# Kernel tuning notes

Measured on AMD Instinct MI355X. Metric: run time of the kernel, lower is better.

## Reference

```python
import jax, jax.numpy as jnp
import numpy as np

NEG_INF = -9e15  # matches -9000000000000000.0 in the torch source


def setup_inputs() -> dict:
    key = jax.random.key(0)
    k1, k2, k3, k4 = jax.random.split(key, 4)
    B, H, N, D = 4, 8, 2048, 64
    queries = jax.random.normal(k1, (B, H, N, D), dtype=jnp.float32)
    keys = jax.random.normal(k2, (B, H, N, D), dtype=jnp.float32)
    values = jax.random.normal(k3, (B, H, N, D), dtype=jnp.float32)
    adj = jax.random.randint(k4, (N, N), 0, 2, dtype=jnp.int32)
    return {"queries": queries, "keys": keys, "values": values, "adj": adj}


def reference(queries, keys, values, adj):
    B, H, N, D = queries.shape
    # e = Q K^T / 8  (hard-coded divisor == sqrt(64))
    e = jnp.einsum("bhnd,bhmd->bhnm", queries, keys) / 8.0
    # graph-adjacency mask (adj [N,N] broadcasts over batch and heads)
    att = jnp.where(adj > 0, e, NEG_INF)
    att = jax.nn.softmax(att, axis=-1)
    # dropout p=0.0 / eval mode -> identity
    h_prime = jnp.einsum("bhnm,bhmd->bhnd", att, values)  # [B,H,N,D]
    # original uses .view (flat reshape), NOT a permute
    return h_prime.reshape(N, B, H, D)
```

## Files before the change

### kernel.cpp

```cpp
#include <hip/hip_runtime.h>
#include <math.h>

typedef short short8 __attribute__((ext_vector_type(8)));
typedef float float4_t __attribute__((ext_vector_type(4)));
typedef unsigned uint2_t __attribute__((ext_vector_type(2)));
typedef unsigned short ushort_t;

#define BH   32
#define N_   2048
#define D_   64
#define NCH  32
#define LDP  72
#define KV_ELEMS (BH * N_ * D_)
#define OFF_VF  (KV_ELEMS * 2)
#define OFF_MSK (KV_ELEMS * 4)
#define QSCALE 0.18033688f

__device__ __forceinline__ unsigned pack_bf16(float a, float b) {
  union { float f; unsigned u; } ua{a}, ub{b};
  return __builtin_amdgcn_perm(ub.u + 0x8000u, ua.u + 0x8000u, 0x07060302u);
}

__global__ __launch_bounds__(256) void prep_kernel(
    const float* __restrict__ K, const float* __restrict__ V,
    const int* __restrict__ adj, ushort_t* __restrict__ Kf,
    ushort_t* __restrict__ Vf, unsigned long long* __restrict__ msk) {
  __shared__ __align__(16) float Tc[64 * 68];
  const int blk = blockIdx.x, t = threadIdx.x;

  if (blk < 2048) {
    const bool isK = blk < 1024;
    const int b = isK ? blk : blk - 1024;
    const float* src = (isK ? K : V) + (b >> 5) * (N_ * D_) + (b & 31) * 64 * D_;
#pragma unroll
    for (int i = 0; i < 4; ++i) {
      int idx = i * 256 + t;
      int row = idx >> 4, c4 = (idx & 15) * 4;
      *(float4_t*)&Tc[row * 68 + c4] = *(const float4_t*)(src + row * D_ + c4);
    }
    __syncthreads();
    ushort_t* dst = (isK ? Kf : Vf) + b * 4096;
#pragma unroll
    for (int e = 0; e < 2; ++e) {
      int u = t * 2 + e;
      int g = u >> 6, lane = u & 63;
      int ks = g >> 2, quad = lane >> 4, l16 = lane & 15;
      float v[8];
      if (isK) {
        int nt = g & 3;
        const float* rp = &Tc[(nt * 16 + l16) * 68 + ks * 32 + quad * 8];
        float4_t a = *(const float4_t*)(rp);
        float4_t bq = *(const float4_t*)(rp + 4);
#pragma unroll
        for (int j = 0; j < 4; ++j) { v[j] = a[j]; v[4 + j] = bq[j]; }
      } else {
        int dt = g & 3, d = dt * 16 + l16;
#pragma unroll
        for (int j = 0; j < 8; ++j) {
          int key = 16 * (j & 3) + ks * 8 + quad * 2 + (j >> 2);
          v[j] = Tc[key * 68 + d];
        }
      }
      union { short8 s; unsigned u4[4]; } h;
      h.u4[0] = pack_bf16(v[0], v[1]); h.u4[1] = pack_bf16(v[2], v[3]);
      h.u4[2] = pack_bf16(v[4], v[5]); h.u4[3] = pack_bf16(v[6], v[7]);
      *(short8*)(dst + u * 8) = h.s;
    }
  } else {
    const int row = (blk - 2048) * 4 + (t >> 6);
    const int lane = t & 63;
    unsigned long long keep = 0;
#pragma unroll 8
    for (int i = 0; i < 32; ++i) {
      int a = adj[row * N_ + i * 64 + lane];
      unsigned long long b = __ballot(a > 0);
      if (lane == i) keep = b;
    }
    if (lane < 32) msk[row * 32 + lane] = keep;
  }
}

__global__ __launch_bounds__(256, 2) void attn_main(
    const float* __restrict__ Q, const ushort_t* __restrict__ Kf,
    const ushort_t* __restrict__ Vf, const unsigned long long* __restrict__ msk,
    float* __restrict__ O) {
  __shared__ __align__(16) ushort_t lds_p[4][2][16 * LDP];

  const int t    = threadIdx.x;
  const int w    = t >> 6;
  const int lane = t & 63;
  const int quad = lane >> 4;
  const int l16  = lane & 15;
  const int bh   = blockIdx.x & (BH - 1);
  const int qt   = blockIdx.x >> 5;
  const int base = bh * (N_ * D_);
  const int qrow0 = qt * 128 + w * 32;

  const ushort_t* Kfb = Kf + (bh * 32) * 4096;
  const ushort_t* Vfb = Vf + (bh * 32) * 4096;
  const unsigned long long* mr[2] = {
    msk + (qrow0 + quad * 4) * 32,
    msk + (qrow0 + 16 + quad * 4) * 32
  };

  short8 qf[2][2];
#pragma unroll
  for (int qg = 0; qg < 2; ++qg)
#pragma unroll
    for (int ks = 0; ks < 2; ++ks) {
      const float* qp = Q + base + (qrow0 + qg * 16 + l16) * D_ + ks * 32 + quad * 8;
      float4_t f0 = *(const float4_t*)(qp);
      float4_t f1 = *(const float4_t*)(qp + 4);
      union { short8 s; unsigned u[4]; } h;
      h.u[0] = pack_bf16(f0[0] * QSCALE, f0[1] * QSCALE);
      h.u[1] = pack_bf16(f0[2] * QSCALE, f0[3] * QSCALE);
      h.u[2] = pack_bf16(f1[0] * QSCALE, f1[1] * QSCALE);
      h.u[3] = pack_bf16(f1[2] * QSCALE, f1[3] * QSCALE);
      qf[qg][ks] = h.s;
    }

  short8 ones;
#pragma unroll
  for (int j = 0; j < 8; ++j) ones[j] = (short)0x3F80;

  float4_t oacc[2][4];
  float4_t osum[2];
#pragma unroll
  for (int qg = 0; qg < 2; ++qg) {
#pragma unroll
    for (int dt = 0; dt < 4; ++dt) oacc[qg][dt] = (float4_t){0.f, 0.f, 0.f, 0.f};
    osum[qg] = (float4_t){0.f, 0.f, 0.f, 0.f};
  }

  const int fo = lane * 8;

  for (int c = 0; c < NCH; ++c) {
    const ushort_t* kg = Kfb + c * 4096;
    const ushort_t* vg = Vfb + c * 4096;

    short8 kfr[2][4], vfr[2][4];
#pragma unroll
    for (int ks = 0; ks < 2; ++ks)
#pragma unroll
      for (int nt = 0; nt < 4; ++nt) {
        kfr[ks][nt] = *(const short8*)(kg + (ks * 4 + nt) * 512 + fo);
        vfr[ks][nt] = *(const short8*)(vg + (ks * 4 + nt) * 512 + fo);
      }
    unsigned long long mw[2][4];
#pragma unroll
    for (int qg = 0; qg < 2; ++qg)
#pragma unroll
      for (int r = 0; r < 4; ++r) mw[qg][r] = mr[qg][r * 32 + c];

#pragma unroll
    for (int qg = 0; qg < 2; ++qg) {
      float4_t sacc[4];
#pragma unroll
      for (int nt = 0; nt < 4; ++nt) sacc[nt] = (float4_t){0.f, 0.f, 0.f, 0.f};
#pragma unroll
      for (int ks = 0; ks < 2; ++ks)
#pragma unroll
        for (int nt = 0; nt < 4; ++nt)
          sacc[nt] = __builtin_amdgcn_mfma_f32_16x16x32_bf16(qf[qg][ks], kfr[ks][nt], sacc[nt], 0, 0, 0);

#pragma unroll
      for (int r = 0; r < 4; ++r) {
        unsigned long long sh = mw[qg][r] >> l16;
        unsigned lo = (unsigned)sh, hi = (unsigned)(sh >> 32);
        float p0 = (lo & 1u)       ? exp2f(sacc[0][r]) : 0.f;
        float p1 = (lo & 0x10000u) ? exp2f(sacc[1][r]) : 0.f;
        float p2 = (hi & 1u)       ? exp2f(sacc[2][r]) : 0.f;
        float p3 = (hi & 0x10000u) ? exp2f(sacc[3][r]) : 0.f;
        uint2_t d2;
        d2.x = pack_bf16(p0, p1);
        d2.y = pack_bf16(p2, p3);
        *(uint2_t*)&lds_p[w][qg][(quad * 4 + r) * LDP + (l16 << 2)] = d2;
      }
    }

#pragma unroll
    for (int qg = 0; qg < 2; ++qg)
#pragma unroll
      for (int ks = 0; ks < 2; ++ks) {
        short8 pf = *(const short8*)&lds_p[w][qg][l16 * LDP + ks * 32 + quad * 8];
#pragma unroll
        for (int dt = 0; dt < 4; ++dt)
          oacc[qg][dt] = __builtin_amdgcn_mfma_f32_16x16x32_bf16(pf, vfr[ks][dt], oacc[qg][dt], 0, 0, 0);
        osum[qg] = __builtin_amdgcn_mfma_f32_16x16x32_bf16(pf, ones, osum[qg], 0, 0, 0);
      }
  }

#pragma unroll
  for (int qg = 0; qg < 2; ++qg)
#pragma unroll
    for (int r = 0; r < 4; ++r) {
      float inv = 1.f / osum[qg][r];
      int qi = qrow0 + qg * 16 + quad * 4 + r;
#pragma unroll
      for (int dt = 0; dt < 4; ++dt)
        O[base + qi * D_ + dt * 16 + l16] = oacc[qg][dt][r] * inv;
    }
}

extern "C" void kernel_launch(void* const* d_in, const int* in_sizes, int n_in,
                              void* d_out, int out_size, void* d_ws, size_t ws_size,
                              hipStream_t stream) {
  const float* Q  = (const float*)d_in[0];
  const float* K  = (const float*)d_in[1];
  const float* V  = (const float*)d_in[2];
  const int* adj  = (const int*)d_in[3];
  float* O        = (float*)d_out;
  ushort_t* Kf    = (ushort_t*)d_ws;
  ushort_t* Vf    = (ushort_t*)((char*)d_ws + OFF_VF);
  unsigned long long* msk = (unsigned long long*)((char*)d_ws + OFF_MSK);

  prep_kernel<<<2560, 256, 0, stream>>>(K, V, adj, Kf, Vf, msk);
  attn_main<<<512, 256, 0, stream>>>(Q, Kf, Vf, msk, O);
}
```

Baseline: 184.3 us.

## Double-buffer K/V chunks in LDS via async global-to-LDS loads shared across waves

Each K/V chunk is now loaded once per block straight into a double-buffered LDS array with global_load_lds. Previously each of the four waves pulled the same chunk from global memory into registers. The next chunk is prefetched while the current one is computed, and the MFMA loops are reordered so each K/V fragment read from LDS feeds both query groups. This cuts redundant global/L2 traffic and hides load latency. The cost is about 32 KB of extra LDS and a block-wide barrier on every chunk.

Result: faster. 175.5 us (-4.7%).

```diff
diff --git a/kernel.cpp b/kernel.cpp
--- a/kernel.cpp
+++ b/kernel.cpp
@@ -19,6 +19,12 @@
 __device__ __forceinline__ unsigned pack_bf16(float a, float b) {
   union { float f; unsigned u; } ua{a}, ub{b};
   return __builtin_amdgcn_perm(ub.u + 0x8000u, ua.u + 0x8000u, 0x07060302u);
+}
+
+__device__ __forceinline__ void gload_lds16(const ushort_t* g, ushort_t* l) {
+  __builtin_amdgcn_global_load_lds(
+      (const __attribute__((address_space(1))) unsigned int*)(g),
+      (__attribute__((address_space(3))) unsigned int*)(l), 16, 0, 0);
 }
 
 __global__ __launch_bounds__(256) void prep_kernel(
@@ -84,6 +90,7 @@
     const float* __restrict__ Q, const ushort_t* __restrict__ Kf,
     const ushort_t* __restrict__ Vf, const unsigned long long* __restrict__ msk,
     float* __restrict__ O) {
+  __shared__ __align__(16) ushort_t kv[2][8192];
   __shared__ __align__(16) ushort_t lds_p[4][2][16 * LDP];
 
   const int t    = threadIdx.x;
@@ -134,60 +141,79 @@
 
   const int fo = lane * 8;
 
+#define STAGE(nb, c)                                                           \
+  do {                                                                         \
+    const ushort_t* _sk = Kfb + (c)*4096 + w * 1024 + lane * 8;                \
+    const ushort_t* _sv = Vfb + (c)*4096 + w * 1024 + lane * 8;                \
+    ushort_t* _dk = &kv[nb][w * 1024];                                         \
+    ushort_t* _dv = &kv[nb][4096 + w * 1024];                                  \
+    gload_lds16(_sk, _dk);                                                     \
+    gload_lds16(_sk + 512, _dk + 512);                                         \
+    gload_lds16(_sv, _dv);                                                     \
+    gload_lds16(_sv + 512, _dv + 512);                                         \
+  } while (0)
+
+  STAGE(0, 0);
+
+#pragma unroll 2
   for (int c = 0; c < NCH; ++c) {
-    const ushort_t* kg = Kfb + c * 4096;
-    const ushort_t* vg = Vfb + c * 4096;
-
-    short8 kfr[2][4], vfr[2][4];
+    const int cur = c & 1;
+    __syncthreads();
+
+    unsigned long long mw[2][4];
+#pragma unroll
+    for (int qg = 0; qg < 2; ++qg)
+#pragma unroll
+      for (int r = 0; r < 4; ++r) mw[qg][r] = mr[qg][r * 32 + c];
+
+    if (c + 1 < NCH) STAGE(cur ^ 1, c + 1);
+
+    const ushort_t* kb = &kv[cur][0];
+    const ushort_t* vb = &kv[cur][4096];
+
+    float4_t sacc[2][4];
+#pragma unroll
+    for (int qg = 0; qg < 2; ++qg)
+#pragma unroll
+      for (int nt = 0; nt < 4; ++nt) sacc[qg][nt] = (float4_t){0.f, 0.f, 0.f, 0.f};
 #pragma unroll
     for (int ks = 0; ks < 2; ++ks)
 #pragma unroll
       for (int nt = 0; nt < 4; ++nt) {
-        kfr[ks][nt] = *(const short8*)(kg + (ks * 4 + nt) * 512 + fo);
-        vfr[ks][nt] = *(const short8*)(vg + (ks * 4 + nt) * 512 + fo);
-      }
-    unsigned long long mw[2][4];
+        short8 kfr = *(const short8*)(kb + (ks * 4 + nt) * 512 + fo);
+        sacc[0][nt] = __builtin_amdgcn_mfma_f32_16x16x32_bf16(qf[0][ks], kfr, sacc[0][nt], 0, 0, 0);
+        sacc[1][nt] = __builtin_amdgcn_mfma_f32_16x16x32_bf16(qf[1][ks], kfr, sacc[1][nt], 0, 0, 0);
+      }
+
 #pragma unroll
     for (int qg = 0; qg < 2; ++qg)
-#pragma unroll
-      for (int r = 0; r < 4; ++r) mw[qg][r] = mr[qg][r * 32 + c];
-
-#pragma unroll
-    for (int qg = 0; qg < 2; ++qg) {
-      float4_t sacc[4];
-#pragma unroll
-      for (int nt = 0; nt < 4; ++nt) sacc[nt] = (float4_t){0.f, 0.f, 0.f, 0.f};
-#pragma unroll
-      for (int ks = 0; ks < 2; ++ks)
-#pragma unroll
-        for (int nt = 0; nt < 4; ++nt)
-          sacc[nt] = __builtin_amdgcn_mfma_f32_16x16x32_bf16(qf[qg][ks], kfr[ks][nt], sacc[nt], 0, 0, 0);
-
 #pragma unroll
       for (int r = 0; r < 4; ++r) {
         unsigned long long sh = mw[qg][r] >> l16;
         unsigned lo = (unsigned)sh, hi = (unsigned)(sh >> 32);
-        float p0 = (lo & 1u)       ? exp2f(sacc[0][r]) : 0.f;
-        float p1 = (lo & 0x10000u) ? exp2f(sacc[1][r]) : 0.f;
-        float p2 = (hi & 1u)       ? exp2f(sacc[2][r]) : 0.f;
-        float p3 = (hi & 0x10000u) ? exp2f(sacc[3][r]) : 0.f;
+        float p0 = (lo & 1u)       ? exp2f(sacc[qg][0][r]) : 0.f;
+        float p1 = (lo & 0x10000u) ? exp2f(sacc[qg][1][r]) : 0.f;
+        float p2 = (hi & 1u)       ? exp2f(sacc[qg][2][r]) : 0.f;
+        float p3 = (hi & 0x10000u) ? exp2f(sacc[qg][3][r]) : 0.f;
         uint2_t d2;
         d2.x = pack_bf16(p0, p1);
         d2.y = pack_bf16(p2, p3);
         *(uint2_t*)&lds_p[w][qg][(quad * 4 + r) * LDP + (l16 << 2)] = d2;
       }
-    }
-
-#pragma unroll
-    for (int qg = 0; qg < 2; ++qg)
-#pragma unroll
-      for (int ks = 0; ks < 2; ++ks) {
-        short8 pf = *(const short8*)&lds_p[w][qg][l16 * LDP + ks * 32 + quad * 8];
-#pragma unroll
-        for (int dt = 0; dt < 4; ++dt)
-          oacc[qg][dt] = __builtin_amdgcn_mfma_f32_16x16x32_bf16(pf, vfr[ks][dt], oacc[qg][dt], 0, 0, 0);
-        osum[qg] = __builtin_amdgcn_mfma_f32_16x16x32_bf16(pf, ones, osum[qg], 0, 0, 0);
-      }
+
+#pragma unroll
+    for (int ks = 0; ks < 2; ++ks) {
+      short8 pf0 = *(const short8*)&lds_p[w][0][l16 * LDP + ks * 32 + quad * 8];
+      short8 pf1 = *(const short8*)&lds_p[w][1][l16 * LDP + ks * 32 + quad * 8];
+#pragma unroll
+      for (int dt = 0; dt < 4; ++dt) {
+        short8 vfr = *(const short8*)(vb + (ks * 4 + dt) * 512 + fo);
+        oacc[0][dt] = __builtin_amdgcn_mfma_f32_16x16x32_bf16(pf0, vfr, oacc[0][dt], 0, 0, 0);
+        oacc[1][dt] = __builtin_amdgcn_mfma_f32_16x16x32_bf16(pf1, vfr, oacc[1][dt], 0, 0, 0);
+      }
+      osum[0] = __builtin_amdgcn_mfma_f32_16x16x32_bf16(pf0, ones, osum[0], 0, 0, 0);
+      osum[1] = __builtin_amdgcn_mfma_f32_16x16x32_bf16(pf1, ones, osum[1], 0, 0, 0);
+    }
   }
 
 #pragma unroll
```
